# Kernel tuning notes

Measured on AMD Instinct MI355X. Metric: run time of the kernel, lower is better.

Reference implementation:

```python
import jax, jax.numpy as jnp
import numpy as np

N_NODES = 20000
N_EDGES = 100000
ATOM_F = 40
BOND_F = 10
H = 32          # n_node_hidden
EH = 128        # n_edge_hidden
N_LAYERS = 3
EPS = 1e-5
NEG_SLOPE = 0.8


def _bn(x, g, b):
    # BatchNorm1d in training mode: batch mean / biased variance over dim 0
    m = x.mean(0)
    v = x.var(0)
    return (x - m) * jax.lax.rsqrt(v + EPS) * g + b


def setup_inputs() -> dict:
    key = jax.random.key(0)
    ks = iter(jax.random.split(key, 32))

    def nrm(shape, scale):
        return jax.random.normal(next(ks), shape, dtype=jnp.float32) * scale

    inp = {
        "x_node": jax.random.normal(next(ks), (N_NODES, ATOM_F), dtype=jnp.float32),
        "x_edge": jax.random.normal(next(ks), (N_EDGES, BOND_F), dtype=jnp.float32),
        "src": jax.random.randint(next(ks), (N_EDGES,), 0, N_NODES, dtype=jnp.int32),
        "dst": jax.random.randint(next(ks), (N_EDGES,), 0, N_NODES, dtype=jnp.int32),
        # Embedding params
        "bn_n_g": jnp.ones((ATOM_F,), jnp.float32),
        "bn_n_b": jnp.zeros((ATOM_F,), jnp.float32),
        "node_W": nrm((ATOM_F, H), 1.0 / np.sqrt(ATOM_F)),
        "node_b": jnp.zeros((H,), jnp.float32),
        "bn_e_g": jnp.ones((BOND_F,), jnp.float32),
        "bn_e_b": jnp.zeros((BOND_F,), jnp.float32),
        "edge_W": nrm((BOND_F, EH), 1.0 / np.sqrt(BOND_F)),
        "edge_b": jnp.zeros((EH,), jnp.float32),
        # Edge-network (NNConv edge_func) params
        "en_W1": nrm((EH, EH), 1.0 / np.sqrt(EH)),
        "en_b1": jnp.zeros((EH,), jnp.float32),
        "en_bn1_g": jnp.ones((EH,), jnp.float32),
        "en_bn1_b": jnp.zeros((EH,), jnp.float32),
        "en_W2": nrm((EH, H * H), 1.0 / np.sqrt(EH)),
        "en_b2": jnp.zeros((H * H,), jnp.float32),
        "en_bn2_g": jnp.ones((H * H,), jnp.float32),
        "en_bn2_b": jnp.zeros((H * H,), jnp.float32),
        # GRU params (torch layout: [3H, in], gate order r,z,n)
        "gru_Wih": nrm((3 * H, H), 1.0 / np.sqrt(H)),
        "gru_Whh": nrm((3 * H, H), 1.0 / np.sqrt(H)),
        "gru_bih": jnp.zeros((3 * H,), jnp.float32),
        "gru_bhh": jnp.zeros((3 * H,), jnp.float32),
    }
    return inp


def reference(x_node, x_edge, src, dst,
              bn_n_g, bn_n_b, node_W, node_b,
              bn_e_g, bn_e_b, edge_W, edge_b,
              en_W1, en_b1, en_bn1_g, en_bn1_b,
              en_W2, en_b2, en_bn2_g, en_bn2_b,
              gru_Wih, gru_Whh, gru_bih, gru_bhh):
    # ---- Embedding ----
    h_node = _bn(x_node, bn_n_g, bn_n_b) @ node_W + node_b          # [N, H]
    h_edge = _bn(x_edge, bn_e_g, bn_e_b) @ edge_W + edge_b          # [E, EH]

    # ---- Edge network (depends only on h_edge; identical every layer) ----
    t = _bn(h_edge @ en_W1 + en_b1, en_bn1_g, en_bn1_b)
    t = jnp.where(t > 0, t, NEG_SLOPE * t)                          # LeakyReLU(0.8)
    W_e = _bn(t @ en_W2 + en_b2, en_bn2_g, en_bn2_b).reshape(-1, H, H)  # [E, H, H]

    # mean-aggregation denominator (zero in-degree -> message stays 0)
    deg = jax.ops.segment_sum(jnp.ones_like(dst, jnp.float32), dst, num_segments=N_NODES)
    denom = jnp.maximum(deg, 1.0)[:, None]                          # [N, 1]

    def gru_cell(x, h):
        gi = x @ gru_Wih.T + gru_bih
        gh = h @ gru_Whh.T + gru_bhh
        gi_r, gi_z, gi_n = jnp.split(gi, 3, axis=-1)
        gh_r, gh_z, gh_n = jnp.split(gh, 3, axis=-1)
        r = jax.nn.sigmoid(gi_r + gh_r)
        z = jax.nn.sigmoid(gi_z + gh_z)
        n = jnp.tanh(gi_n + r * gh_n)
        return (1.0 - z) * n + z * h

    h = h_node
    for _ in range(N_LAYERS):
        msg = jnp.einsum('ei,eio->eo', h[src], W_e)                 # per-edge matmul
        m = jax.ops.segment_sum(msg, dst, num_segments=N_NODES) / denom  # scatter-mean
        h = gru_cell(m, h)
    return h
```

## Files before the change

### kernel.cpp

```cpp
#include <hip/hip_runtime.h>
#include <hip/hip_fp16.h>

#define NN 20000
#define NE 100000
#define TSQ_NB 256

typedef _Float16 f16x8 __attribute__((ext_vector_type(8)));
typedef float f32x4 __attribute__((ext_vector_type(4)));

__device__ __forceinline__ float wred(float v) {
#pragma unroll
  for (int k = 1; k < 64; k <<= 1) v += __shfl_xor(v, k);
  return v;
}

__global__ void zerok(float* __restrict__ p, int n) {
  int i = blockIdx.x * 256 + threadIdx.x;
  if (i < n) p[i] = 0.f;
}

template <int C>
__global__ void colstats(const float* __restrict__ x, float* __restrict__ stat, int total) {
  __shared__ float ls[2 * C];
  for (int i = threadIdx.x; i < 2 * C; i += blockDim.x) ls[i] = 0.f;
  __syncthreads();
  for (int idx = blockIdx.x * blockDim.x + threadIdx.x; idx < total; idx += gridDim.x * blockDim.x) {
    float v = x[idx];
    int c = idx % C;
    atomicAdd(&ls[c], v);
    atomicAdd(&ls[C + c], v * v);
  }
  __syncthreads();
  for (int i = threadIdx.x; i < 2 * C; i += blockDim.x) atomicAdd(&stat[i], ls[i]);
}

__global__ void finalize_bn(const float* __restrict__ stat, const float* __restrict__ g,
                            const float* __restrict__ b, float* __restrict__ s_out,
                            float* __restrict__ c_out, int C, float invR) {
  int c = blockIdx.x * blockDim.x + threadIdx.x;
  if (c >= C) return;
  float mean = stat[c] * invR;
  float var = fmaxf(stat[C + c] * invR - mean * mean, 0.f);
  float sc = g[c] * rsqrtf(var + 1e-5f);
  s_out[c] = sc;
  c_out[c] = b[c] - mean * sc;
}

__global__ void deg_kernel(const int* __restrict__ dst, float* __restrict__ deg, int E) {
  int e = blockIdx.x * blockDim.x + threadIdx.x;
  if (e < E) atomicAdd(&deg[dst[e]], 1.f);
}

__global__ void invden_kernel(const float* __restrict__ deg, float* __restrict__ inv, int N) {
  int n = blockIdx.x * blockDim.x + threadIdx.x;
  if (n < N) inv[n] = 1.f / fmaxf(deg[n], 1.f);
}

__global__ void fold_w1(const float* __restrict__ edge_W, const float* __restrict__ edge_b,
                        const float* __restrict__ en_W1, const float* __restrict__ en_b1,
                        float* __restrict__ Wc, float* __restrict__ bc) {
  int t = threadIdx.x;
  for (int idx = t; idx < 1280; idx += 256) {
    int bq = idx >> 7, j = idx & 127;
    float a = 0.f;
    for (int q = 0; q < 128; ++q) a += edge_W[bq * 128 + q] * en_W1[q * 128 + j];
    Wc[idx] = a;
  }
  if (t < 128) {
    float a = en_b1[t];
    for (int q = 0; q < 128; ++q) a += edge_b[q] * en_W1[q * 128 + t];
    bc[t] = a;
  }
}

__global__ __launch_bounds__(64) void sx_kernel(const float* __restrict__ x,
                                                const float* __restrict__ es,
                                                const float* __restrict__ ec,
                                                float* __restrict__ sxs, int E) {
  float s[10][10], xs[10], esl[10], ecl[10];
#pragma unroll
  for (int a = 0; a < 10; ++a) {
    xs[a] = 0.f; esl[a] = es[a]; ecl[a] = ec[a];
#pragma unroll
    for (int b = 0; b < 10; ++b) s[a][b] = 0.f;
  }
  for (int e = blockIdx.x * 64 + threadIdx.x; e < E; e += gridDim.x * 64) {
    float xb[10];
#pragma unroll
    for (int q = 0; q < 10; ++q) xb[q] = x[(size_t)e * 10 + q] * esl[q] + ecl[q];
#pragma unroll
    for (int a = 0; a < 10; ++a) {
      xs[a] += xb[a];
#pragma unroll
      for (int b = 0; b < 10; ++b) s[a][b] += xb[a] * xb[b];
    }
  }
#pragma unroll
  for (int a = 0; a < 10; ++a) {
    float r = wred(xs[a]);
    if (threadIdx.x == 0) atomicAdd(&sxs[100 + a], r);
#pragma unroll
    for (int b = 0; b < 10; ++b) {
      float r2 = wred(s[a][b]);
      if (threadIdx.x == 0) atomicAdd(&sxs[a * 10 + b], r2);
    }
  }
}

__global__ void bn1_from_sx(const float* __restrict__ sxs, const float* __restrict__ Wc,
                            const float* __restrict__ bc, const float* __restrict__ g,
                            const float* __restrict__ b, float* __restrict__ s1,
                            float* __restrict__ c1) {
  int j = threadIdx.x;
  float w[10];
#pragma unroll
  for (int q = 0; q < 10; ++q) w[q] = Wc[q * 128 + j];
  float d = 0.f;
#pragma unroll
  for (int q = 0; q < 10; ++q) d += sxs[100 + q] * w[q];
  float qq = 0.f;
#pragma unroll
  for (int a = 0; a < 10; ++a) {
    float p = 0.f;
#pragma unroll
    for (int bq = 0; bq < 10; ++bq) p += sxs[a * 10 + bq] * w[bq];
    qq += w[a] * p;
  }
  float invE = 1.f / (float)NE;
  float bias = bc[j];
  float mean = d * invE + bias;
  float m2 = (qq + 2.f * bias * d) * invE + bias * bias;
  float var = fmaxf(m2 - mean * mean, 0.f);
  float sc = g[j] * rsqrtf(var + 1e-5f);
  s1[j] = sc;
  c1[j] = b[j] - mean * sc;
}

__global__ __launch_bounds__(256) void t_kernel(const float* __restrict__ x,
                                                const float* __restrict__ es,
                                                const float* __restrict__ ec,
                                                const float* __restrict__ Wc,
                                                const float* __restrict__ bcb,
                                                const float* __restrict__ s1,
                                                const float* __restrict__ c1,
                                                __half* __restrict__ T, int E) {
  __shared__ float Wcl[1280], bcl[128], s1l[128], c1l[128], esl[10], ecl[10];
  __shared__ float xr[16][10];
  int t = threadIdx.x;
  for (int i = t; i < 1280; i += 256) Wcl[i] = Wc[i];
  if (t < 128) { bcl[t] = bcb[t]; s1l[t] = s1[t]; c1l[t] = c1[t]; }
  if (t < 10) { esl[t] = es[t]; ecl[t] = ec[t]; }
  int r0 = blockIdx.x * 16;
  if (t < 160) xr[t / 10][t % 10] = x[(size_t)r0 * 10 + t];
  __syncthreads();
  int rl = t >> 4, c0 = (t & 15) * 8;
  float acc[8];
#pragma unroll
  for (int j = 0; j < 8; ++j) acc[j] = bcl[c0 + j];
#pragma unroll
  for (int q = 0; q < 10; ++q) {
    float xb = xr[rl][q] * esl[q] + ecl[q];
#pragma unroll
    for (int j = 0; j < 8; ++j) acc[j] += xb * Wcl[q * 128 + c0 + j];
  }
  f16x8 o;
#pragma unroll
  for (int j = 0; j < 8; ++j) {
    float tv = acc[j] * s1l[c0 + j] + c1l[c0 + j];
    tv = tv > 0.f ? tv : 0.8f * tv;
    o[j] = (_Float16)tv;
  }
  *(f16x8*)&T[(size_t)(r0 + rl) * 128 + c0] = o;
}

__global__ __launch_bounds__(256) void colsum_t(const __half* __restrict__ T,
                                                float* __restrict__ tsum, int E) {
  __shared__ float cs[128];
  int t = threadIdx.x;
  int col = t & 127, hf = t >> 7;
  float a = 0.f;
  for (int r = blockIdx.x * 2 + hf; r < E; r += gridDim.x * 2)
    a += __half2float(T[(size_t)r * 128 + col]);
  if (hf) cs[col] = a;
  __syncthreads();
  if (!hf) atomicAdd(&tsum[col], a + cs[col]);
}

__global__ __launch_bounds__(256) void tsq_mfma(const __half* __restrict__ T,
                                                float* __restrict__ partial, int E) {
  __shared__ _Float16 tl[32 * 132];
  int t = threadIdx.x;
  int w = t >> 6, lane = t & 63;
  int g = lane >> 4, cl = lane & 15;
  f32x4 acc[2][8];
#pragma unroll
  for (int i = 0; i < 2; ++i)
#pragma unroll
    for (int j = 0; j < 8; ++j) acc[i][j] = {0.f, 0.f, 0.f, 0.f};
  int nch = E >> 5;
  for (int ch = blockIdx.x; ch < nch; ch += gridDim.x) {
    __syncthreads();
#pragma unroll
    for (int p = 0; p < 4; ++p) {
      int u = p * 256 + t;
      int e = u >> 5, c0 = (u & 31) * 4;
      *(uint2*)&tl[e * 132 + c0] = *(const uint2*)&T[((size_t)ch * 32 + e) * 128 + c0];
    }
    __syncthreads();
    f16x8 fr[8];
#pragma unroll
    for (int cb = 0; cb < 8; ++cb) {
      f16x8 f;
#pragma unroll
      for (int j = 0; j < 8; ++j) f[j] = tl[(g * 8 + j) * 132 + cb * 16 + cl];
      fr[cb] = f;
    }
    f16x8 afr[2];
#pragma unroll
    for (int ri = 0; ri < 2; ++ri) {
      int cb = w * 2 + ri;
      f16x8 f;
#pragma unroll
      for (int j = 0; j < 8; ++j) f[j] = tl[(g * 8 + j) * 132 + cb * 16 + cl];
      afr[ri] = f;
    }
#pragma unroll
    for (int ri = 0; ri < 2; ++ri)
#pragma unroll
      for (int ci = 0; ci < 8; ++ci)
        acc[ri][ci] = __builtin_amdgcn_mfma_f32_16x16x32_f16(afr[ri], fr[ci], acc[ri][ci], 0, 0, 0);
  }
  float* pb = partial + (size_t)blockIdx.x * 16384;
#pragma unroll
  for (int ri = 0; ri < 2; ++ri)
#pragma unroll
    for (int ci = 0; ci < 8; ++ci)
#pragma unroll
      for (int q = 0; q < 4; ++q)
        pb[(w * 32 + ri * 16 + g * 4 + q) * 128 + ci * 16 + cl] = acc[ri][ci][q];
}

__global__ void tsq_reduce(const float* __restrict__ partial, float* __restrict__ S) {
  int i = blockIdx.x * 256 + threadIdx.x;
  float a = 0.f;
  for (int b = 0; b < TSQ_NB; ++b) a += partial[(size_t)b * 16384 + i];
  S[i] = a;
}

__global__ __launch_bounds__(256) void bn2p(const float* __restrict__ S,
                                            const float* __restrict__ tsum,
                                            const float* __restrict__ W2,
                                            const float* __restrict__ b2,
                                            const float* __restrict__ g,
                                            const float* __restrict__ b,
                                            float* __restrict__ s2, float* __restrict__ c2p) {
  __shared__ float Sl[16384];
  __shared__ float tsl[128];
  for (int i = threadIdx.x; i < 16384; i += 256) Sl[i] = S[i];
  if (threadIdx.x < 128) tsl[threadIdx.x] = tsum[threadIdx.x];
  __syncthreads();
  int w = threadIdx.x >> 6, lane = threadIdx.x & 63;
  int io = blockIdx.x * 4 + w;
  float wlo = W2[(size_t)lane * 1024 + io];
  float whi = W2[(size_t)(lane + 64) * 1024 + io];
  float plo = 0.f, phi = 0.f;
#pragma unroll
  for (int a = 0; a < 64; ++a) {
    float wa = __shfl(wlo, a);
    plo += wa * Sl[a * 128 + lane];
    phi += wa * Sl[a * 128 + lane + 64];
  }
#pragma unroll
  for (int a = 0; a < 64; ++a) {
    float wa = __shfl(whi, a);
    plo += wa * Sl[(a + 64) * 128 + lane];
    phi += wa * Sl[(a + 64) * 128 + lane + 64];
  }
  float qq = wred(plo * wlo + phi * whi);
  float d = wred(wlo * tsl[lane] + whi * tsl[lane + 64]);
  if (lane == 0) {
    float invE = 1.f / (float)NE;
    float mean_raw = d * invE;
    float var = fmaxf(qq * invE - mean_raw * mean_raw, 0.f);
    float sc = g[io] * rsqrtf(var + 1e-5f);
    s2[io] = sc;
    c2p[io] = b[io] - (mean_raw + b2[io]) * sc;
  }
}

__global__ void repack_w2s(const float* __restrict__ W2, const float* __restrict__ s2,
                           unsigned short* __restrict__ Bp) {
  int idx = blockIdx.x * 256 + threadIdx.x;
  if (idx >= 16384) return;
  int cb = idx >> 8;
  int ks = (idx >> 6) & 3;
  int lane = idx & 63;
  int col = cb * 16 + (lane & 15);
  int kbase = ks * 32 + (lane >> 4) * 8;
  float sc = s2[col];
  unsigned short tmp[8];
#pragma unroll
  for (int j = 0; j < 8; ++j)
    tmp[j] = __half_as_ushort(__float2half(W2[(size_t)(kbase + j) * 1024 + col] * sc));
  *(uint4*)&Bp[(size_t)idx * 8] = *(uint4*)tmp;
}

__global__ __launch_bounds__(256) void layer_prep(const float* __restrict__ h,
                                                  const float* __restrict__ c2p,
                                                  float* __restrict__ hc,
                                                  float* __restrict__ m, int N) {
  __shared__ float cl[1024];
  for (int i = threadIdx.x; i < 1024; i += 256) cl[i] = c2p[i];
  __syncthreads();
  int gid = blockIdx.x * 256 + threadIdx.x;
  if (gid >= N * 32) return;
  int n = gid >> 5, o = gid & 31;
  float a = 0.f;
#pragma unroll
  for (int i = 0; i < 32; ++i) a += h[(size_t)n * 32 + i] * cl[i * 32 + o];
  hc[gid] = a;
  m[gid] = 0.f;
}

__global__ __launch_bounds__(256, 3) void msg_mfma(const __half* __restrict__ T,
                                                   const unsigned short* __restrict__ Bp,
                                                   const float* __restrict__ h,
                                                   const float* __restrict__ hc,
                                                   const int* __restrict__ src,
                                                   const int* __restrict__ dst,
                                                   float* __restrict__ m, int E) {
  __shared__ float hst[32 * 36];
  __shared__ float msw[4 * 1056];
  int t = threadIdx.x;
  int w = t >> 6, lane = t & 63;
  int arow = lane & 15, kgrp = lane >> 4;
  int e0 = blockIdx.x * 32;
  {
    int row = t >> 3, i0 = (t & 7) * 4;
    int e = e0 + row;
    int sn = (e < E) ? src[e] : 0;
    float4 hv = *(const float4*)&h[(size_t)sn * 32 + i0];
    hst[(i0 + 0) * 36 + row] = hv.x;
    hst[(i0 + 1) * 36 + row] = hv.y;
    hst[(i0 + 2) * 36 + row] = hv.z;
    hst[(i0 + 3) * 36 + row] = hv.w;
  }
  __syncthreads();
  f16x8 ah[4][2];
#pragma unroll
  for (int ks = 0; ks < 4; ++ks)
#pragma unroll
    for (int ri = 0; ri < 2; ++ri) {
      int r = e0 + ri * 16 + arow;
      f16x8 av{};
      if (r < E) av = *(const f16x8*)&T[(size_t)r * 128 + ks * 32 + kgrp * 8];
      ah[ks][ri] = av;
    }
  f32x4 pm[2][2];
#pragma unroll
  for (int p = 0; p < 2; ++p)
#pragma unroll
    for (int ri = 0; ri < 2; ++ri) pm[p][ri] = {0.f, 0.f, 0.f, 0.f};
#pragma unroll
  for (int cb = 0; cb < 4; ++cb) {
    f32x4 acc[2][4];
#pragma unroll
    for (int i = 0; i < 2; ++i)
#pragma unroll
      for (int j = 0; j < 4; ++j) acc[i][j] = {0.f, 0.f, 0.f, 0.f};
#pragma unroll
    for (int ks = 0; ks < 4; ++ks) {
#pragma unroll
      for (int ci = 0; ci < 4; ++ci) {
        int f = cb * 16 + w * 4 + ci;
        f16x8 bv = *(const f16x8*)&Bp[((size_t)(f * 4 + ks) * 64 + lane) * 8];
        acc[0][ci] = __builtin_amdgcn_mfma_f32_16x16x32_f16(ah[ks][0], bv, acc[0][ci], 0, 0, 0);
        acc[1][ci] = __builtin_amdgcn_mfma_f32_16x16x32_f16(ah[ks][1], bv, acc[1][ci], 0, 0, 0);
      }
    }
#pragma unroll
    for (int ci = 0; ci < 4; ++ci) {
      int i = cb * 8 + w * 2 + (ci >> 1);
#pragma unroll
      for (int ri = 0; ri < 2; ++ri) {
        f32x4 hv = *(const f32x4*)&hst[i * 36 + ri * 16 + kgrp * 4];
        if (ci & 1) pm[1][ri] += hv * acc[ri][ci];
        else        pm[0][ri] += hv * acc[ri][ci];
      }
    }
  }
  {
    float* mw = &msw[w * 1056];
#pragma unroll
    for (int p = 0; p < 2; ++p) {
      int o = p * 16 + arow;
#pragma unroll
      for (int ri = 0; ri < 2; ++ri) {
        int rb = ri * 16 + kgrp * 4;
        mw[o * 33 + rb + 0] = pm[p][ri][0];
        mw[o * 33 + rb + 1] = pm[p][ri][1];
        mw[o * 33 + rb + 2] = pm[p][ri][2];
        mw[o * 33 + rb + 3] = pm[p][ri][3];
      }
    }
  }
  __syncthreads();
  {
    int row = t >> 3, o0 = (t & 7) * 4;
    int e = e0 + row;
    if (e < E) {
      int sn = src[e], dn = dst[e];
      float* mp = m + (size_t)dn * 32;
      const float* hcp = hc + (size_t)sn * 32;
#pragma unroll
      for (int j = 0; j < 4; ++j) {
        int o = o0 + j;
        float v = msw[0 * 1056 + o * 33 + row] + msw[1 * 1056 + o * 33 + row] +
                  msw[2 * 1056 + o * 33 + row] + msw[3 * 1056 + o * 33 + row];
        v += hcp[o];
        atomicAdd(&mp[o], v);
      }
    }
  }
}

template <int K, int COUT>
__global__ __launch_bounds__(256) void embed_gemm(const float* __restrict__ x,
                                                  const float* __restrict__ s,
                                                  const float* __restrict__ c,
                                                  const float* __restrict__ W,
                                                  const float* __restrict__ bias,
                                                  float* __restrict__ out, int R) {
  __shared__ float Wl[K * COUT];
  __shared__ float sl[K], cl[K];
  for (int i = threadIdx.x; i < K * COUT; i += 256) Wl[i] = W[i];
  for (int i = threadIdx.x; i < K; i += 256) { sl[i] = s[i]; cl[i] = c[i]; }
  __syncthreads();
  int gid = blockIdx.x * 256 + threadIdx.x;
  if (gid >= R * COUT) return;
  int r = gid / COUT, j = gid % COUT;
  float acc = bias[j];
#pragma unroll
  for (int k = 0; k < K; ++k) acc += (x[(size_t)r * K + k] * sl[k] + cl[k]) * Wl[k * COUT + j];
  out[gid] = acc;
}

__global__ __launch_bounds__(256) void gru_kernel(const float* __restrict__ m,
                                                  const float* __restrict__ inv_den,
                                                  const float* __restrict__ h_in,
                                                  const float* __restrict__ Wih,
                                                  const float* __restrict__ Whh,
                                                  const float* __restrict__ bih,
                                                  const float* __restrict__ bhh,
                                                  float* __restrict__ h_out, int N) {
  __shared__ float WT[32 * 96], UT[32 * 96];
  for (int idx = threadIdx.x; idx < 96 * 32; idx += 256) {
    int j = idx / 32, i = idx % 32;
    WT[i * 96 + j] = Wih[idx];
    UT[i * 96 + j] = Whh[idx];
  }
  __syncthreads();
  int gid = blockIdx.x * 256 + threadIdx.x;
  if (gid >= N * 32) return;
  int n = gid >> 5, o = gid & 31;
  float inv = inv_den[n];
  float air = 0.f, aiz = 0.f, ain = 0.f, ahr = 0.f, ahz = 0.f, ahn = 0.f;
#pragma unroll
  for (int i = 0; i < 32; ++i) {
    float mi = m[(size_t)n * 32 + i] * inv;
    float hi = h_in[(size_t)n * 32 + i];
    const float* w = &WT[i * 96 + o];
    const float* u = &UT[i * 96 + o];
    air += mi * w[0];  aiz += mi * w[32];  ain += mi * w[64];
    ahr += hi * u[0];  ahz += hi * u[32];  ahn += hi * u[64];
  }
  float r = 1.f / (1.f + expf(-(air + bih[o] + ahr + bhh[o])));
  float z = 1.f / (1.f + expf(-(aiz + bih[o + 32] + ahz + bhh[o + 32])));
  float ng = tanhf(ain + bih[o + 64] + r * (ahn + bhh[o + 64]));
  h_out[gid] = (1.f - z) * ng + z * h_in[(size_t)n * 32 + o];
}

extern "C" void kernel_launch(void* const* d_in, const int* in_sizes, int n_in,
                              void* d_out, int out_size, void* d_ws, size_t ws_size,
                              hipStream_t stream) {
  const float* x_node = (const float*)d_in[0];
  const float* x_edge = (const float*)d_in[1];
  const int* src = (const int*)d_in[2];
  const int* dst = (const int*)d_in[3];
  const float* bn_n_g = (const float*)d_in[4];
  const float* bn_n_b = (const float*)d_in[5];
  const float* node_W = (const float*)d_in[6];
  const float* node_b = (const float*)d_in[7];
  const float* bn_e_g = (const float*)d_in[8];
  const float* bn_e_b = (const float*)d_in[9];
  const float* edge_W = (const float*)d_in[10];
  const float* edge_b = (const float*)d_in[11];
  const float* en_W1 = (const float*)d_in[12];
  const float* en_b1 = (const float*)d_in[13];
  const float* en_bn1_g = (const float*)d_in[14];
  const float* en_bn1_b = (const float*)d_in[15];
  const float* en_W2 = (const float*)d_in[16];
  const float* en_b2 = (const float*)d_in[17];
  const float* en_bn2_g = (const float*)d_in[18];
  const float* en_bn2_b = (const float*)d_in[19];
  const float* gWih = (const float*)d_in[20];
  const float* gWhh = (const float*)d_in[21];
  const float* gbih = (const float*)d_in[22];
  const float* gbhh = (const float*)d_in[23];
  float* out = (float*)d_out;

  char* ws = (char*)d_ws;
  __half* Tt      = (__half*)(ws + 0);
  float* tsq_part = (float*)(ws + 25600000);
  float* h_a      = (float*)(ws + 42377216);
  float* h_b      = (float*)(ws + 44937216);
  float* m_buf    = (float*)(ws + 47497216);
  float* hc       = (float*)(ws + 50057216);
  float* inv_den  = (float*)(ws + 52617216);
  float* zbase    = (float*)(ws + 52697216);
  float* deg   = zbase;
  float* S     = zbase + 20000;
  float* tsum  = zbase + 36384;
  float* sxs   = zbase + 36512;
  float* nstat = zbase + 36640;
  float* estat = zbase + 36768;
  float* par   = (float*)(ws + 52844800);
  float* ns = par + 0;    float* nc = par + 64;
  float* es = par + 128;  float* ec = par + 192;
  float* s1 = par + 256;  float* c1 = par + 384;
  float* wc = par + 512;
  float* bcb = par + 1792;
  float* s2 = par + 1920; float* c2p = par + 2944;
  unsigned short* Bp = (unsigned short*)(ws + 52861184);

  zerok<<<(36896 + 255) / 256, 256, 0, stream>>>(zbase, 36896);

  colstats<40><<<200, 256, 0, stream>>>(x_node, nstat, NN * 40);
  colstats<10><<<256, 256, 0, stream>>>(x_edge, estat, NE * 10);
  deg_kernel<<<(NE + 255) / 256, 256, 0, stream>>>(dst, deg, NE);
  finalize_bn<<<1, 64, 0, stream>>>(nstat, bn_n_g, bn_n_b, ns, nc, 40, 1.f / NN);
  finalize_bn<<<1, 64, 0, stream>>>(estat, bn_e_g, bn_e_b, es, ec, 10, 1.f / NE);
  invden_kernel<<<(NN + 255) / 256, 256, 0, stream>>>(deg, inv_den, NN);

  fold_w1<<<1, 256, 0, stream>>>(edge_W, edge_b, en_W1, en_b1, wc, bcb);
  sx_kernel<<<128, 64, 0, stream>>>(x_edge, es, ec, sxs, NE);
  bn1_from_sx<<<1, 128, 0, stream>>>(sxs, wc, bcb, en_bn1_g, en_bn1_b, s1, c1);
  t_kernel<<<NE / 16, 256, 0, stream>>>(x_edge, es, ec, wc, bcb, s1, c1, Tt, NE);

  colsum_t<<<512, 256, 0, stream>>>(Tt, tsum, NE);
  tsq_mfma<<<TSQ_NB, 256, 0, stream>>>(Tt, tsq_part, NE);
  tsq_reduce<<<64, 256, 0, stream>>>(tsq_part, S);
  bn2p<<<256, 256, 0, stream>>>(S, tsum, en_W2, en_b2, en_bn2_g, en_bn2_b, s2, c2p);

  embed_gemm<40, 32><<<(NN * 32 + 255) / 256, 256, 0, stream>>>(x_node, ns, nc, node_W, node_b, h_a, NN);
  repack_w2s<<<64, 256, 0, stream>>>(en_W2, s2, Bp);

  const float* hin = h_a;
  for (int l = 0; l < 3; ++l) {
    float* hout = (l == 0) ? h_b : (l == 1) ? h_a : out;
    layer_prep<<<(NN * 32 + 255) / 256, 256, 0, stream>>>(hin, c2p, hc, m_buf, NN);
    msg_mfma<<<(NE + 31) / 32, 256, 0, stream>>>(Tt, Bp, hin, hc, src, dst, m_buf, NE);
    gru_kernel<<<(NN * 32 + 255) / 256, 256, 0, stream>>>(m_buf, inv_den, hin, gWih, gWhh,
                                                          gbih, gbhh, hout, NN);
    hin = hout;
  }
}
```

Measured before the change: 627.8 us.

## Fuse next-layer prep into GRU kernel, drop bounds checks, raise msg occupancy

The per-layer hc projection and m zeroing, previously done in layer_prep, now run at the end of gru_kernel for the following layer. Only the first layer keeps a standalone layer_prep launch, which removes two launches and one re-read of h. The edge-count bounds checks are removed from msg_mfma and gru_kernel, relying on the fixed sizes dividing evenly by the block sizes. msg_mfma's launch-bounds occupancy hint rises from 3 to 6 blocks, which caps registers per thread and may cause spills in the MFMA accumulator loop.

```diff
diff --git a/kernel.cpp b/kernel.cpp
--- a/kernel.cpp
+++ b/kernel.cpp
@@ -322,7 +322,7 @@
   m[gid] = 0.f;
 }
 
-__global__ __launch_bounds__(256, 3) void msg_mfma(const __half* __restrict__ T,
+__global__ __launch_bounds__(256, 6) void msg_mfma(const __half* __restrict__ T,
                                                    const unsigned short* __restrict__ Bp,
                                                    const float* __restrict__ h,
                                                    const float* __restrict__ hc,
@@ -337,8 +337,7 @@
   int e0 = blockIdx.x * 32;
   {
     int row = t >> 3, i0 = (t & 7) * 4;
-    int e = e0 + row;
-    int sn = (e < E) ? src[e] : 0;
+    int sn = src[e0 + row];
     float4 hv = *(const float4*)&h[(size_t)sn * 32 + i0];
     hst[(i0 + 0) * 36 + row] = hv.x;
     hst[(i0 + 1) * 36 + row] = hv.y;
@@ -350,12 +349,8 @@
 #pragma unroll
   for (int ks = 0; ks < 4; ++ks)
 #pragma unroll
-    for (int ri = 0; ri < 2; ++ri) {
-      int r = e0 + ri * 16 + arow;
-      f16x8 av{};
-      if (r < E) av = *(const f16x8*)&T[(size_t)r * 128 + ks * 32 + kgrp * 8];
-      ah[ks][ri] = av;
-    }
+    for (int ri = 0; ri < 2; ++ri)
+      ah[ks][ri] = *(const f16x8*)&T[(size_t)(e0 + ri * 16 + arow) * 128 + ks * 32 + kgrp * 8];
   f32x4 pm[2][2];
 #pragma unroll
   for (int p = 0; p < 2; ++p)
@@ -408,18 +403,16 @@
   {
     int row = t >> 3, o0 = (t & 7) * 4;
     int e = e0 + row;
-    if (e < E) {
-      int sn = src[e], dn = dst[e];
-      float* mp = m + (size_t)dn * 32;
-      const float* hcp = hc + (size_t)sn * 32;
-#pragma unroll
-      for (int j = 0; j < 4; ++j) {
-        int o = o0 + j;
-        float v = msw[0 * 1056 + o * 33 + row] + msw[1 * 1056 + o * 33 + row] +
-                  msw[2 * 1056 + o * 33 + row] + msw[3 * 1056 + o * 33 + row];
-        v += hcp[o];
-        atomicAdd(&mp[o], v);
-      }
+    int sn = src[e], dn = dst[e];
+    float* mp = m + (size_t)dn * 32;
+    const float* hcp = hc + (size_t)sn * 32;
+#pragma unroll
+    for (int j = 0; j < 4; ++j) {
+      int o = o0 + j;
+      float v = msw[0 * 1056 + o * 33 + row] + msw[1 * 1056 + o * 33 + row] +
+                msw[2 * 1056 + o * 33 + row] + msw[3 * 1056 + o * 33 + row];
+      v += hcp[o];
+      atomicAdd(&mp[o], v);
     }
   }
 }
@@ -452,16 +445,24 @@
                                                   const float* __restrict__ Whh,
                                                   const float* __restrict__ bih,
                                                   const float* __restrict__ bhh,
-                                                  float* __restrict__ h_out, int N) {
+                                                  float* __restrict__ h_out,
+                                                  const float* __restrict__ c2p,
+                                                  float* __restrict__ hc_out,
+                                                  float* __restrict__ m_next,
+                                                  int do_next, int N) {
   __shared__ float WT[32 * 96], UT[32 * 96];
-  for (int idx = threadIdx.x; idx < 96 * 32; idx += 256) {
+  __shared__ float c2l[1024];
+  __shared__ float hnew[256];
+  int t = threadIdx.x;
+  for (int idx = t; idx < 96 * 32; idx += 256) {
     int j = idx / 32, i = idx % 32;
     WT[i * 96 + j] = Wih[idx];
     UT[i * 96 + j] = Whh[idx];
   }
-  __syncthreads();
-  int gid = blockIdx.x * 256 + threadIdx.x;
-  if (gid >= N * 32) return;
+  if (do_next)
+    for (int i = t; i < 1024; i += 256) c2l[i] = c2p[i];
+  __syncthreads();
+  int gid = blockIdx.x * 256 + t;
   int n = gid >> 5, o = gid & 31;
   float inv = inv_den[n];
   float air = 0.f, aiz = 0.f, ain = 0.f, ahr = 0.f, ahz = 0.f, ahn = 0.f;
@@ -477,7 +478,18 @@
   float r = 1.f / (1.f + expf(-(air + bih[o] + ahr + bhh[o])));
   float z = 1.f / (1.f + expf(-(aiz + bih[o + 32] + ahz + bhh[o + 32])));
   float ng = tanhf(ain + bih[o + 64] + r * (ahn + bhh[o + 64]));
-  h_out[gid] = (1.f - z) * ng + z * h_in[(size_t)n * 32 + o];
+  float hval = (1.f - z) * ng + z * h_in[(size_t)n * 32 + o];
+  h_out[gid] = hval;
+  if (do_next) {
+    hnew[t] = hval;
+    __syncthreads();
+    int nl = t >> 5;
+    float a = 0.f;
+#pragma unroll
+    for (int i = 0; i < 32; ++i) a += hnew[nl * 32 + i] * c2l[i * 32 + o];
+    hc_out[gid] = a;
+    m_next[gid] = 0.f;
+  }
 }
 
 extern "C" void kernel_launch(void* const* d_in, const int* in_sizes, int n_in,
@@ -555,13 +567,15 @@
   embed_gemm<40, 32><<<(NN * 32 + 255) / 256, 256, 0, stream>>>(x_node, ns, nc, node_W, node_b, h_a, NN);
   repack_w2s<<<64, 256, 0, stream>>>(en_W2, s2, Bp);
 
+  layer_prep<<<(NN * 32 + 255) / 256, 256, 0, stream>>>(h_a, c2p, hc, m_buf, NN);
+
   const float* hin = h_a;
   for (int l = 0; l < 3; ++l) {
     float* hout = (l == 0) ? h_b : (l == 1) ? h_a : out;
-    layer_prep<<<(NN * 32 + 255) / 256, 256, 0, stream>>>(hin, c2p, hc, m_buf, NN);
-    msg_mfma<<<(NE + 31) / 32, 256, 0, stream>>>(Tt, Bp, hin, hc, src, dst, m_buf, NE);
+    msg_mfma<<<NE / 32, 256, 0, stream>>>(Tt, Bp, hin, hc, src, dst, m_buf, NE);
     gru_kernel<<<(NN * 32 + 255) / 256, 256, 0, stream>>>(m_buf, inv_den, hin, gWih, gWhh,
-                                                          gbih, gbhh, hout, NN);
+                                                          gbih, gbhh, hout, c2p, hc, m_buf,
+                                                          (l < 2) ? 1 : 0, NN);
     hin = hout;
   }
 }
```

Result: slower. 1.978 ms (+215.0%).
